# Kernel tuning notes

Measured on AMD Instinct MI355X. Metric: run time of the kernel, lower is better.

Reference implementation:

```python
import jax, jax.numpy as jnp
import numpy as np

EPS = 1e-06

def feature_map(x):
    # ELU + 1 feature map (default in LinearAttention)
    return jax.nn.elu(x) + 1.0

def setup_inputs() -> dict:
    key = jax.random.key(0)
    kq, kk, kv = jax.random.split(key, 3)
    N, L, H, D = 4, 8192, 16, 64
    queries = jax.random.normal(kq, (N, L, H, D), dtype=jnp.float32)
    keys = jax.random.normal(kk, (N, L, H, D), dtype=jnp.float32)
    values = jax.random.normal(kv, (N, L, H, D), dtype=jnp.float32)
    return {"queries": queries, "keys": keys, "values": values}

def reference(queries, keys, values):
    # Q, K: [N, L, H, D] after ELU+1 feature map
    Q = feature_map(queries)
    K = feature_map(keys)
    # KV state: [N, H, D, M]
    KV = jnp.einsum('nshd,nshm->nhdm', K, values)
    # normalizer: Z[n,l,h] = 1 / (Q . sum_s K + eps)
    Z = 1.0 / (jnp.einsum('nlhd,nhd->nlh', Q, K.sum(axis=1)) + EPS)
    # NOTE: faithful to original: KV (nhdm) is labeled 'nhmd' in the einsum,
    # i.e. KV is used transposed on its last two axes (requires D == M).
    V = jnp.einsum('nlhd,nhmd,nlh->nlhm', Q, KV, Z)
    return V
```

## Files before the change

### kernel.cpp

```cpp
#include <hip/hip_runtime.h>
#include <hip/hip_bf16.h>

#define LDIM 8192
#define HDIM 16
#define DDIM 64
#define NHEADPAIR 64
#define ROWSTRIDE 1024
#define KVSZ 4160
#define EPSF 1e-6f
#define TROWS 32

typedef float f32x4 __attribute__((ext_vector_type(4)));
typedef short s16x8 __attribute__((ext_vector_type(8)));

__device__ __forceinline__ float featmap(float x) {
    return x > 0.0f ? x + 1.0f : __expf(x);
}

__device__ __forceinline__ unsigned int pack_bf16x2(float a, float b) {
    union { __hip_bfloat162 h; unsigned int u; } x;
    x.h = __float22bfloat162_rn(make_float2(a, b));
    return x.u;
}

__device__ __forceinline__ int swz(int d) { return ((d >> 3) & 3) << 2; }

__global__ __launch_bounds__(256) void kv_mfma_kernel(
    const float* __restrict__ Kp, const float* __restrict__ Vp,
    float* __restrict__ part, int chunks, int rowsPerBlock)
{
    __shared__ unsigned int KT[2][64 * 16];
    __shared__ unsigned int VT[2][64 * 16];

    const int nh   = blockIdx.x;
    const int ch   = blockIdx.y;
    const int n    = nh >> 4;
    const int h    = nh & 15;
    const int t    = threadIdx.x;
    const int wave = t >> 6;
    const int lane = t & 63;

    const size_t base = (((size_t)n * LDIM) * HDIM + h) * DDIM
                      + (size_t)ch * rowsPerBlock * ROWSTRIDE;

    const bool isK = (t < 128);
    const int  u   = t & 127;
    const int  dg  = u & 7;
    const int  rp  = u >> 3;
    const float* Sb = (isK ? Kp : Vp) + base + (size_t)(2 * rp) * ROWSTRIDE + dg * 8;

    const int NT = rowsPerBlock / TROWS;

    f32x4 acc[4];
    f32x4 zac;
#pragma unroll
    for (int mt = 0; mt < 4; ++mt) acc[mt] = (f32x4){0.f, 0.f, 0.f, 0.f};
    zac = (f32x4){0.f, 0.f, 0.f, 0.f};

    s16x8 ones;
#pragma unroll
    for (int i = 0; i < 8; ++i) ones[i] = (short)0x3F80;

    const int fr = lane & 15;
    const int fk = lane >> 4;
    const int d0 = wave * 16;
    const int raddr = (d0 + fr) * 16 + ((fk * 4) ^ swz(d0 + fr));

    float4 a0, a1, b0, b1;
    a0 = *(const float4*)(Sb);
    a1 = *(const float4*)(Sb + 4);
    b0 = *(const float4*)(Sb + ROWSTRIDE);
    b1 = *(const float4*)(Sb + ROWSTRIDE + 4);
    {
        unsigned int* T = isK ? &KT[0][0] : &VT[0][0];
        float fa[8] = { a0.x, a0.y, a0.z, a0.w, a1.x, a1.y, a1.z, a1.w };
        float fb[8] = { b0.x, b0.y, b0.z, b0.w, b1.x, b1.y, b1.z, b1.w };
        if (isK) {
#pragma unroll
            for (int j = 0; j < 8; ++j) { fa[j] = featmap(fa[j]); fb[j] = featmap(fb[j]); }
        }
#pragma unroll
        for (int j = 0; j < 8; ++j) {
            const int d = dg * 8 + j;
            T[d * 16 + (rp ^ swz(d))] = pack_bf16x2(fa[j], fb[j]);
        }
    }
    __syncthreads();

    int buf = 0;
    for (int tt = 0; tt < NT; ++tt) {
        const bool more = (tt + 1 < NT);
        if (more) {
            const float* S = Sb + (size_t)(tt + 1) * TROWS * ROWSTRIDE;
            a0 = *(const float4*)(S);
            a1 = *(const float4*)(S + 4);
            b0 = *(const float4*)(S + ROWSTRIDE);
            b1 = *(const float4*)(S + ROWSTRIDE + 4);
        }

        {
            s16x8 A = *(const s16x8*)&KT[buf][raddr];
            zac = __builtin_amdgcn_mfma_f32_16x16x32_bf16(A, ones, zac, 0, 0, 0);
#pragma unroll
            for (int mt = 0; mt < 4; ++mt) {
                const int m = mt * 16 + fr;
                s16x8 B = *(const s16x8*)&VT[buf][m * 16 + ((fk * 4) ^ swz(m))];
                acc[mt] = __builtin_amdgcn_mfma_f32_16x16x32_bf16(A, B, acc[mt], 0, 0, 0);
            }
        }

        if (more) {
            unsigned int* T = isK ? &KT[buf ^ 1][0] : &VT[buf ^ 1][0];
            float fa[8] = { a0.x, a0.y, a0.z, a0.w, a1.x, a1.y, a1.z, a1.w };
            float fb[8] = { b0.x, b0.y, b0.z, b0.w, b1.x, b1.y, b1.z, b1.w };
            if (isK) {
#pragma unroll
                for (int j = 0; j < 8; ++j) { fa[j] = featmap(fa[j]); fb[j] = featmap(fb[j]); }
            }
#pragma unroll
            for (int j = 0; j < 8; ++j) {
                const int d = dg * 8 + j;
                T[d * 16 + (rp ^ swz(d))] = pack_bf16x2(fa[j], fb[j]);
            }
        }
        __syncthreads();
        buf ^= 1;
    }

    float* p = part + (size_t)(nh * chunks + ch) * KVSZ;
#pragma unroll
    for (int mt = 0; mt < 4; ++mt) {
#pragma unroll
        for (int reg = 0; reg < 4; ++reg) {
            p[(d0 + fk * 4 + reg) * 64 + mt * 16 + fr] = acc[mt][reg];
        }
    }
    if (fr == 0) {
#pragma unroll
        for (int reg = 0; reg < 4; ++reg)
            p[4096 + d0 + fk * 4 + reg] = zac[reg];
    }
}

__global__ __launch_bounds__(256) void kv_reduce_kernel(
    const float* __restrict__ part, unsigned short* __restrict__ kvh, int chunks)
{
    const int nh = blockIdx.y;
    const int e  = blockIdx.x * 256 + threadIdx.x;
    if (e >= KVSZ) return;
    float s = 0.0f;
    for (int c = 0; c < chunks; ++c)
        s += part[(size_t)(nh * chunks + c) * KVSZ + e];
    union { __hip_bfloat16 h; unsigned short u; } cv;
    cv.h = __float2bfloat16(s);
    kvh[(size_t)nh * KVSZ + e] = cv.u;
}

__global__ __launch_bounds__(256) void attn_mfma_kernel(
    const float* __restrict__ Qp, const unsigned short* __restrict__ kvh,
    float* __restrict__ out)
{
    __shared__ unsigned int kvU[64][36];
    __shared__ unsigned int ksU[36];
    __shared__ unsigned int qU[128][36];

    const int nh = blockIdx.y;
    const int n  = nh >> 4;
    const int h  = nh & 15;
    const int t  = threadIdx.x;

    {
        const unsigned int* kvg = (const unsigned int*)(kvh + (size_t)nh * KVSZ);
        const int r  = t >> 2;
        const int c0 = (t & 3) * 8;
        uint4 x = *(const uint4*)(kvg + r * 32 + c0);
        uint4 y = *(const uint4*)(kvg + r * 32 + c0 + 4);
        *(uint4*)&kvU[r][c0]     = x;
        *(uint4*)&kvU[r][c0 + 4] = y;
        if (t < 32) ksU[t] = kvg[2048 + t];
    }

    {
        const int qr = t >> 1;
        const float* qg = Qp + ((((size_t)n * LDIM) + (size_t)blockIdx.x * 128 + qr)
                                * HDIM + h) * DDIM + (t & 1) * 32;
        unsigned int q[16];
#pragma unroll
        for (int j = 0; j < 8; ++j) {
            float4 f = *(const float4*)(qg + j * 4);
            q[2 * j]     = pack_bf16x2(featmap(f.x), featmap(f.y));
            q[2 * j + 1] = pack_bf16x2(featmap(f.z), featmap(f.w));
        }
        uint4* dst = (uint4*)&qU[qr][(t & 1) * 16];
        dst[0] = make_uint4(q[0],  q[1],  q[2],  q[3]);
        dst[1] = make_uint4(q[4],  q[5],  q[6],  q[7]);
        dst[2] = make_uint4(q[8],  q[9],  q[10], q[11]);
        dst[3] = make_uint4(q[12], q[13], q[14], q[15]);
    }
    __syncthreads();

    const int wave = t >> 6;
    const int lane = t & 63;
    const int fr = lane & 15;
    const int fk = lane >> 4;

    s16x8 bF[4][2], kF[2];
#pragma unroll
    for (int mt = 0; mt < 4; ++mt)
#pragma unroll
        for (int kk = 0; kk < 2; ++kk)
            bF[mt][kk] = *(const s16x8*)&kvU[mt * 16 + fr][kk * 16 + fk * 4];
#pragma unroll
    for (int kk = 0; kk < 2; ++kk)
        kF[kk] = *(const s16x8*)&ksU[kk * 16 + fk * 4];

    f32x4 acc[2][4];
    f32x4 zac[2];
#pragma unroll
    for (int lt = 0; lt < 2; ++lt) {
        zac[lt] = (f32x4){0.f, 0.f, 0.f, 0.f};
#pragma unroll
        for (int mt = 0; mt < 4; ++mt) acc[lt][mt] = (f32x4){0.f, 0.f, 0.f, 0.f};
    }

#pragma unroll
    for (int kk = 0; kk < 2; ++kk) {
#pragma unroll
        for (int lt = 0; lt < 2; ++lt) {
            s16x8 A = *(const s16x8*)&qU[wave * 32 + lt * 16 + fr][kk * 16 + fk * 4];
            zac[lt] = __builtin_amdgcn_mfma_f32_16x16x32_bf16(A, kF[kk], zac[lt], 0, 0, 0);
#pragma unroll
            for (int mt = 0; mt < 4; ++mt)
                acc[lt][mt] = __builtin_amdgcn_mfma_f32_16x16x32_bf16(
                    A, bF[mt][kk], acc[lt][mt], 0, 0, 0);
        }
    }

#pragma unroll
    for (int lt = 0; lt < 2; ++lt) {
#pragma unroll
        for (int reg = 0; reg < 4; ++reg) {
            const int row = blockIdx.x * 128 + wave * 32 + lt * 16 + fk * 4 + reg;
            const float z = 1.0f / (zac[lt][reg] + EPSF);
            float* orow = out + (((size_t)n * LDIM + row) * HDIM + h) * DDIM;
#pragma unroll
            for (int mt = 0; mt < 4; ++mt)
                orow[mt * 16 + fr] = acc[lt][mt][reg] * z;
        }
    }
}

extern "C" void kernel_launch(void* const* d_in, const int* in_sizes, int n_in,
                              void* d_out, int out_size, void* d_ws, size_t ws_size,
                              hipStream_t stream) {
    const float* Q = (const float*)d_in[0];
    const float* K = (const float*)d_in[1];
    const float* V = (const float*)d_in[2];
    float* out = (float*)d_out;
    float* ws  = (float*)d_ws;

    int chunks = 32;
    while (chunks > 4 &&
           (size_t)NHEADPAIR * chunks * KVSZ * sizeof(float)
             + (size_t)NHEADPAIR * KVSZ * sizeof(unsigned short) > ws_size)
        chunks >>= 1;
    const int rowsPerBlock = LDIM / chunks;

    float* part = ws;
    unsigned short* kvh = (unsigned short*)(ws + (size_t)NHEADPAIR * chunks * KVSZ);

    dim3 g1(NHEADPAIR, chunks);
    kv_mfma_kernel<<<g1, 256, 0, stream>>>(K, V, part, chunks, rowsPerBlock);
    dim3 gr((KVSZ + 255) / 256, NHEADPAIR);
    kv_reduce_kernel<<<gr, 256, 0, stream>>>(part, kvh, chunks);
    dim3 g2(LDIM / 128, NHEADPAIR);
    attn_mfma_kernel<<<g2, 256, 0, stream>>>(Q, kvh, out);
}
```

Before: 146.1 us.

## Process four heads per KV block so each wave owns a full head

The KV accumulation kernel now handles four consecutive heads per block, with one head per wave computing the full 64x64 KV tile. Each thread loads four heads' 64-float row segments, so reads cover contiguous 1 KB spans of K/V rows instead of 256 B per head. The grid shrinks from 64x32 to 16x32 blocks. Per-wave accumulators grow to 16 MFMA tiles, which raises register and LDS pressure and cuts the number of blocks in flight. The chunk count is hardcoded to 32 and the workspace-size fallback is dropped.

```diff
diff --git a/kernel.cpp b/kernel.cpp
--- a/kernel.cpp
+++ b/kernel.cpp
@@ -9,6 +9,9 @@
 #define KVSZ 4160
 #define EPSF 1e-6f
 #define TROWS 32
+#define CHUNKS 32
+#define RPB 256
+#define NT 8
 
 typedef float f32x4 __attribute__((ext_vector_type(4)));
 typedef short s16x8 __attribute__((ext_vector_type(8)));
@@ -27,62 +30,63 @@
 
 __global__ __launch_bounds__(256) void kv_mfma_kernel(
     const float* __restrict__ Kp, const float* __restrict__ Vp,
-    float* __restrict__ part, int chunks, int rowsPerBlock)
+    float* __restrict__ part)
 {
-    __shared__ unsigned int KT[2][64 * 16];
-    __shared__ unsigned int VT[2][64 * 16];
-
-    const int nh   = blockIdx.x;
+    __shared__ unsigned int KT[2][4][1024];
+    __shared__ unsigned int VT[2][4][1024];
+
+    const int bq   = blockIdx.x;
+    const int n    = bq >> 2;
+    const int hq   = bq & 3;
     const int ch   = blockIdx.y;
-    const int n    = nh >> 4;
-    const int h    = nh & 15;
     const int t    = threadIdx.x;
     const int wave = t >> 6;
     const int lane = t & 63;
-
-    const size_t base = (((size_t)n * LDIM) * HDIM + h) * DDIM
-                      + (size_t)ch * rowsPerBlock * ROWSTRIDE;
 
     const bool isK = (t < 128);
     const int  u   = t & 127;
     const int  dg  = u & 7;
     const int  rp  = u >> 3;
-    const float* Sb = (isK ? Kp : Vp) + base + (size_t)(2 * rp) * ROWSTRIDE + dg * 8;
-
-    const int NT = rowsPerBlock / TROWS;
-
-    f32x4 acc[4];
-    f32x4 zac;
-#pragma unroll
-    for (int mt = 0; mt < 4; ++mt) acc[mt] = (f32x4){0.f, 0.f, 0.f, 0.f};
-    zac = (f32x4){0.f, 0.f, 0.f, 0.f};
-
-    s16x8 ones;
-#pragma unroll
-    for (int i = 0; i < 8; ++i) ones[i] = (short)0x3F80;
+    const float* Sp = isK ? Kp : Vp;
+    const size_t base0 = (((size_t)n * LDIM + (size_t)ch * RPB + 2 * rp) * ROWSTRIDE)
+                       + hq * 256 + dg * 8;
 
     const int fr = lane & 15;
     const int fk = lane >> 4;
-    const int d0 = wave * 16;
-    const int raddr = (d0 + fr) * 16 + ((fk * 4) ^ swz(d0 + fr));
-
-    float4 a0, a1, b0, b1;
-    a0 = *(const float4*)(Sb);
-    a1 = *(const float4*)(Sb + 4);
-    b0 = *(const float4*)(Sb + ROWSTRIDE);
-    b1 = *(const float4*)(Sb + ROWSTRIDE + 4);
-    {
-        unsigned int* T = isK ? &KT[0][0] : &VT[0][0];
-        float fa[8] = { a0.x, a0.y, a0.z, a0.w, a1.x, a1.y, a1.z, a1.w };
-        float fb[8] = { b0.x, b0.y, b0.z, b0.w, b1.x, b1.y, b1.z, b1.w };
-        if (isK) {
-#pragma unroll
-            for (int j = 0; j < 8; ++j) { fa[j] = featmap(fa[j]); fb[j] = featmap(fb[j]); }
-        }
+
+    f32x4 acc[4][4];
+    f32x4 zac[4];
+#pragma unroll
+    for (int b = 0; b < 4; ++b) {
+        zac[b] = (f32x4){0.f, 0.f, 0.f, 0.f};
+#pragma unroll
+        for (int mb = 0; mb < 4; ++mb) acc[b][mb] = (f32x4){0.f, 0.f, 0.f, 0.f};
+    }
+    s16x8 ones;
+#pragma unroll
+    for (int i = 0; i < 8; ++i) ones[i] = (short)0x3F80;
+
+    float4 st[4][4];
+
+#pragma unroll
+    for (int hh = 0; hh < 4; ++hh) {
+        const float* S = Sp + base0 + hh * 64;
+        st[hh][0] = *(const float4*)(S);
+        st[hh][1] = *(const float4*)(S + 4);
+        st[hh][2] = *(const float4*)(S + ROWSTRIDE);
+        st[hh][3] = *(const float4*)(S + ROWSTRIDE + 4);
+    }
+#pragma unroll
+    for (int hh = 0; hh < 4; ++hh) {
+        unsigned int* T = isK ? &KT[0][hh][0] : &VT[0][hh][0];
+        const float* a = (const float*)&st[hh][0];
+        const float* b = (const float*)&st[hh][2];
 #pragma unroll
         for (int j = 0; j < 8; ++j) {
             const int d = dg * 8 + j;
-            T[d * 16 + (rp ^ swz(d))] = pack_bf16x2(fa[j], fb[j]);
+            float fe = a[j], fo = b[j];
+            if (isK) { fe = featmap(fe); fo = featmap(fo); }
+            T[d * 16 + (rp ^ swz(d))] = pack_bf16x2(fe, fo);
         }
     }
     __syncthreads();
@@ -91,66 +95,82 @@
     for (int tt = 0; tt < NT; ++tt) {
         const bool more = (tt + 1 < NT);
         if (more) {
-            const float* S = Sb + (size_t)(tt + 1) * TROWS * ROWSTRIDE;
-            a0 = *(const float4*)(S);
-            a1 = *(const float4*)(S + 4);
-            b0 = *(const float4*)(S + ROWSTRIDE);
-            b1 = *(const float4*)(S + ROWSTRIDE + 4);
+#pragma unroll
+            for (int hh = 0; hh < 4; ++hh) {
+                const float* S = Sp + base0
+                               + (size_t)(tt + 1) * TROWS * ROWSTRIDE + hh * 64;
+                st[hh][0] = *(const float4*)(S);
+                st[hh][1] = *(const float4*)(S + 4);
+                st[hh][2] = *(const float4*)(S + ROWSTRIDE);
+                st[hh][3] = *(const float4*)(S + ROWSTRIDE + 4);
+            }
         }
 
         {
-            s16x8 A = *(const s16x8*)&KT[buf][raddr];
-            zac = __builtin_amdgcn_mfma_f32_16x16x32_bf16(A, ones, zac, 0, 0, 0);
-#pragma unroll
-            for (int mt = 0; mt < 4; ++mt) {
-                const int m = mt * 16 + fr;
-                s16x8 B = *(const s16x8*)&VT[buf][m * 16 + ((fk * 4) ^ swz(m))];
-                acc[mt] = __builtin_amdgcn_mfma_f32_16x16x32_bf16(A, B, acc[mt], 0, 0, 0);
+            s16x8 A[4];
+#pragma unroll
+            for (int b = 0; b < 4; ++b) {
+                const int d = b * 16 + fr;
+                A[b] = *(const s16x8*)&KT[buf][wave][d * 16 + ((fk * 4) ^ swz(d))];
+            }
+#pragma unroll
+            for (int b = 0; b < 4; ++b)
+                zac[b] = __builtin_amdgcn_mfma_f32_16x16x32_bf16(A[b], ones, zac[b], 0, 0, 0);
+#pragma unroll
+            for (int mb = 0; mb < 4; ++mb) {
+                const int m = mb * 16 + fr;
+                s16x8 B = *(const s16x8*)&VT[buf][wave][m * 16 + ((fk * 4) ^ swz(m))];
+#pragma unroll
+                for (int b = 0; b < 4; ++b)
+                    acc[b][mb] = __builtin_amdgcn_mfma_f32_16x16x32_bf16(A[b], B, acc[b][mb], 0, 0, 0);
             }
         }
 
         if (more) {
-            unsigned int* T = isK ? &KT[buf ^ 1][0] : &VT[buf ^ 1][0];
-            float fa[8] = { a0.x, a0.y, a0.z, a0.w, a1.x, a1.y, a1.z, a1.w };
-            float fb[8] = { b0.x, b0.y, b0.z, b0.w, b1.x, b1.y, b1.z, b1.w };
-            if (isK) {
-#pragma unroll
-                for (int j = 0; j < 8; ++j) { fa[j] = featmap(fa[j]); fb[j] = featmap(fb[j]); }
-            }
-#pragma unroll
-            for (int j = 0; j < 8; ++j) {
-                const int d = dg * 8 + j;
-                T[d * 16 + (rp ^ swz(d))] = pack_bf16x2(fa[j], fb[j]);
+#pragma unroll
+            for (int hh = 0; hh < 4; ++hh) {
+                unsigned int* T = isK ? &KT[buf ^ 1][hh][0] : &VT[buf ^ 1][hh][0];
+                const float* a = (const float*)&st[hh][0];
+                const float* b = (const float*)&st[hh][2];
+#pragma unroll
+                for (int j = 0; j < 8; ++j) {
+                    const int d = dg * 8 + j;
+                    float fe = a[j], fo = b[j];
+                    if (isK) { fe = featmap(fe); fo = featmap(fo); }
+                    T[d * 16 + (rp ^ swz(d))] = pack_bf16x2(fe, fo);
+                }
             }
         }
         __syncthreads();
         buf ^= 1;
     }
 
-    float* p = part + (size_t)(nh * chunks + ch) * KVSZ;
-#pragma unroll
-    for (int mt = 0; mt < 4; ++mt) {
-#pragma unroll
-        for (int reg = 0; reg < 4; ++reg) {
-            p[(d0 + fk * 4 + reg) * 64 + mt * 16 + fr] = acc[mt][reg];
-        }
-    }
-    if (fr == 0) {
-#pragma unroll
-        for (int reg = 0; reg < 4; ++reg)
-            p[4096 + d0 + fk * 4 + reg] = zac[reg];
-    }
+    const int nh = n * 16 + hq * 4 + wave;
+    float* p = part + ((size_t)nh * CHUNKS + ch) * KVSZ;
+#pragma unroll
+    for (int b = 0; b < 4; ++b)
+#pragma unroll
+        for (int mb = 0; mb < 4; ++mb)
+#pragma unroll
+            for (int reg = 0; reg < 4; ++reg)
+                p[(b * 16 + fk * 4 + reg) * 64 + mb * 16 + fr] = acc[b][mb][reg];
+    if (fr == 0)
+#pragma unroll
+        for (int b = 0; b < 4; ++b)
+#pragma unroll
+            for (int reg = 0; reg < 4; ++reg)
+                p[4096 + b * 16 + fk * 4 + reg] = zac[b][reg];
 }
 
 __global__ __launch_bounds__(256) void kv_reduce_kernel(
-    const float* __restrict__ part, unsigned short* __restrict__ kvh, int chunks)
+    const float* __restrict__ part, unsigned short* __restrict__ kvh)
 {
     const int nh = blockIdx.y;
     const int e  = blockIdx.x * 256 + threadIdx.x;
     if (e >= KVSZ) return;
     float s = 0.0f;
-    for (int c = 0; c < chunks; ++c)
-        s += part[(size_t)(nh * chunks + c) * KVSZ + e];
+    for (int c = 0; c < CHUNKS; ++c)
+        s += part[((size_t)nh * CHUNKS + c) * KVSZ + e];
     union { __hip_bfloat16 h; unsigned short u; } cv;
     cv.h = __float2bfloat16(s);
     kvh[(size_t)nh * KVSZ + e] = cv.u;
@@ -259,20 +279,13 @@
     float* out = (float*)d_out;
     float* ws  = (float*)d_ws;
 
-    int chunks = 32;
-    while (chunks > 4 &&
-           (size_t)NHEADPAIR * chunks * KVSZ * sizeof(float)
-             + (size_t)NHEADPAIR * KVSZ * sizeof(unsigned short) > ws_size)
-        chunks >>= 1;
-    const int rowsPerBlock = LDIM / chunks;
-
     float* part = ws;
-    unsigned short* kvh = (unsigned short*)(ws + (size_t)NHEADPAIR * chunks * KVSZ);
-
-    dim3 g1(NHEADPAIR, chunks);
-    kv_mfma_kernel<<<g1, 256, 0, stream>>>(K, V, part, chunks, rowsPerBlock);
+    unsigned short* kvh = (unsigned short*)(ws + (size_t)NHEADPAIR * CHUNKS * KVSZ);
+
+    dim3 g1(16, CHUNKS);
+    kv_mfma_kernel<<<g1, 256, 0, stream>>>(K, V, part);
     dim3 gr((KVSZ + 255) / 256, NHEADPAIR);
-    kv_reduce_kernel<<<gr, 256, 0, stream>>>(part, kvh, chunks);
+    kv_reduce_kernel<<<gr, 256, 0, stream>>>(part, kvh);
     dim3 g2(LDIM / 128, NHEADPAIR);
     attn_mfma_kernel<<<g2, 256, 0, stream>>>(Q, kvh, out);
 }
```

After: 149.8 us. 2.5% more time.
